# Kernel tuning notes

Measured on AMD Instinct MI355X. Metric: run time of the kernel, lower is better.

Reference implementation:

```python
import jax, jax.numpy as jnp
import numpy as np

DIM = 512
NUM_HEADS = 8
NUM_BLOCKS = 16
# NOTE: original code computes head_dim from FULL dim (before the reduce layer),
# so scale = (dim // num_heads) ** -0.5 = 64 ** -0.5, even though the actual
# per-head dim after reduce is 32. We preserve this quirk faithfully.
SCALE = (DIM // NUM_HEADS) ** -0.5


def setup_inputs() -> dict:
    key = jax.random.key(0)
    ks = jax.random.split(key, 5)
    B, N = 4, 4096
    C = DIM // 2
    x = jax.random.normal(ks[0], (B, N, DIM), dtype=jnp.float32)
    reduce_w = jax.random.normal(ks[1], (DIM, C), dtype=jnp.float32) * (DIM ** -0.5)
    qkv_w = jax.random.normal(ks[2], (C, 3 * C), dtype=jnp.float32) * (C ** -0.5)
    proj_w = jax.random.normal(ks[3], (C, DIM), dtype=jnp.float32) * (C ** -0.5)
    proj_b = jnp.zeros((DIM,), dtype=jnp.float32)
    return {"x": x, "reduce_w": reduce_w, "qkv_w": qkv_w,
            "proj_w": proj_w, "proj_b": proj_b}


def reference(x, reduce_w, qkv_w, proj_w, proj_b):
    B, N, _ = x.shape
    xr = x @ reduce_w                      # [B, N, C]  (C = dim/2)
    C = xr.shape[-1]
    H = NUM_HEADS
    d = C // H
    qkv = (xr @ qkv_w).reshape(B, N, 3, H, d).transpose(2, 0, 3, 1, 4)  # [3,B,H,N,d]
    q, k, v = qkv[0], qkv[1], qkv[2]
    bs = N // NUM_BLOCKS                   # block (chunk) size
    # block-diagonal local attention: reshape seq into independent blocks
    qb = q.reshape(B, H, NUM_BLOCKS, bs, d)
    kb = k.reshape(B, H, NUM_BLOCKS, bs, d)
    vb = v.reshape(B, H, NUM_BLOCKS, bs, d)
    attn = jnp.einsum('bhnqd,bhnkd->bhnqk', qb, kb) * SCALE
    attn = jax.nn.softmax(attn, axis=-1)
    ob = jnp.einsum('bhnqk,bhnkd->bhnqd', attn, vb)   # [B,H,Nb,bs,d]
    # torch: per-block transpose(1,2) then cat on dim=1 -> [B, N, H, d]
    o = ob.transpose(0, 2, 3, 1, 4).reshape(B, N, C)
    return o @ proj_w + proj_b
```

## Files before the change

kernel.cpp:

```cpp
#include <hip/hip_runtime.h>
#include <hip/hip_fp16.h>

typedef _Float16 half_t;
typedef _Float16 f16x8 __attribute__((ext_vector_type(8)));
typedef __fp16 fp16x2 __attribute__((ext_vector_type(2)));
typedef float f32x4 __attribute__((ext_vector_type(4)));

#define MFMA_F16(a, b, c) __builtin_amdgcn_mfma_f32_16x16x32_f16((a), (b), (c), 0, 0, 0)

static __device__ inline unsigned pkrtz(float a, float b) {
    union { fp16x2 h; unsigned u; } c;
    c.h = __builtin_amdgcn_cvt_pkrtz(a, b);
    return c.u;
}

__device__ __forceinline__ void gload16(const half_t* g, half_t* l) {
    __builtin_amdgcn_global_load_lds(
        (const __attribute__((address_space(1))) void*)g,
        (__attribute__((address_space(3))) void*)l, 16, 0, 0);
}

__global__ __launch_bounds__(256) void prep(
    const float* __restrict__ x, const float* __restrict__ qw,
    const float* __restrict__ rw, const float* __restrict__ pw,
    half_t* __restrict__ x_h, half_t* __restrict__ pw_t, half_t* __restrict__ Wt) {
    __shared__ __align__(16) char smem[24576];
    const int bid = blockIdx.x, tid = threadIdx.x;

    if (bid < 48) {
        char* As = smem;
        char* Bs = smem + 8192;
        const int M0 = (bid % 12) * 64, N0 = (bid / 12) * 128;
        const int lane = tid & 63, w = tid >> 6;
        const int l15 = lane & 15, l4 = lane >> 4;
        const int wrow = (w >> 1) * 32, wcol = (w & 1) * 64;
        const int pa = (l15 & 7) << 4;

        f32x4 acc[2][4];
#pragma unroll
        for (int i = 0; i < 2; ++i)
#pragma unroll
            for (int j = 0; j < 4; ++j) acc[i][j] = (f32x4){0.f, 0.f, 0.f, 0.f};

        for (int kc = 0; kc < 4; ++kc) {
            int c0 = kc * 64;
            __syncthreads();
#pragma unroll
            for (int i = 0; i < 2; ++i) {
                int j = tid + i * 256;
                int row = j >> 3, e8 = (j & 7) * 8;
                float s = (M0 + row) < 256 ? 0.125f : 1.f;
                f16x8 v;
#pragma unroll
                for (int e = 0; e < 8; ++e)
                    v[e] = (half_t)(qw[(size_t)(c0 + e8 + e) * 768 + M0 + row] * s);
                *(f16x8*)(As + row * 128 + ((e8 * 2) ^ ((row & 7) << 4))) = v;
            }
#pragma unroll
            for (int i = 0; i < 4; ++i) {
                int j = tid + i * 256;
                int row = j >> 3, e8 = (j & 7) * 8;
                const float* p = rw + (size_t)(N0 + row) * 256 + c0 + e8;
                float4 u0 = *(const float4*)p;
                float4 u1 = *(const float4*)(p + 4);
                f16x8 v;
                v[0] = (half_t)u0.x; v[1] = (half_t)u0.y;
                v[2] = (half_t)u0.z; v[3] = (half_t)u0.w;
                v[4] = (half_t)u1.x; v[5] = (half_t)u1.y;
                v[6] = (half_t)u1.z; v[7] = (half_t)u1.w;
                *(f16x8*)(Bs + row * 128 + ((e8 * 2) ^ ((row & 7) << 4))) = v;
            }
            __syncthreads();
#pragma unroll
            for (int ki = 0; ki < 2; ++ki) {
                f16x8 af[2], bf[4];
#pragma unroll
                for (int mi = 0; mi < 2; ++mi) {
                    int row = wrow + mi * 16 + l15;
                    af[mi] = *(const f16x8*)(As + row * 128 + (((ki * 4 + l4) << 4) ^ pa));
                }
#pragma unroll
                for (int nj = 0; nj < 4; ++nj) {
                    int row = wcol + nj * 16 + l15;
                    bf[nj] = *(const f16x8*)(Bs + row * 128 + (((ki * 4 + l4) << 4) ^ pa));
                }
#pragma unroll
                for (int mi = 0; mi < 2; ++mi)
#pragma unroll
                    for (int nj = 0; nj < 4; ++nj)
                        acc[mi][nj] = MFMA_F16(af[mi], bf[nj], acc[mi][nj]);
            }
        }
#pragma unroll
        for (int mi = 0; mi < 2; ++mi)
#pragma unroll
            for (int nj = 0; nj < 4; ++nj)
#pragma unroll
                for (int reg = 0; reg < 4; ++reg) {
                    int grow = M0 + wrow + mi * 16 + l4 * 4 + reg;
                    int gcol = N0 + wcol + nj * 16 + l15;
                    Wt[(size_t)grow * 512 + gcol] = (half_t)acc[mi][nj][reg];
                }
        return;
    }

    if (bid < 80) {
        half_t* tile = (half_t*)smem;
        int t = bid - 48;
        int R0 = (t >> 3) * 64, C0 = (t & 7) * 64;
#pragma unroll
        for (int e = 0; e < 16; ++e) {
            int idx = tid + e * 256;
            int r = idx >> 6, c = idx & 63;
            tile[r * 72 + c] = (half_t)pw[(size_t)(R0 + r) * 512 + C0 + c];
        }
        __syncthreads();
#pragma unroll
        for (int e = 0; e < 16; ++e) {
            int idx = tid + e * 256;
            int c = idx >> 6, r = idx & 63;
            pw_t[(size_t)(C0 + c) * 256 + R0 + r] = tile[r * 72 + c];
        }
        return;
    }

    int i8 = ((bid - 80) * 256 + tid) * 8;
    float4 a = *(const float4*)(x + i8);
    float4 b = *(const float4*)(x + i8 + 4);
    f16x8 v;
    v[0] = (half_t)a.x; v[1] = (half_t)a.y; v[2] = (half_t)a.z; v[3] = (half_t)a.w;
    v[4] = (half_t)b.x; v[5] = (half_t)b.y; v[6] = (half_t)b.z; v[7] = (half_t)b.w;
    *(f16x8*)(x_h + i8) = v;
}

template <int EPI, int K, int NB>
__global__ __launch_bounds__(256) void gemm_f16(
    const half_t* __restrict__ A, const half_t* __restrict__ Bt,
    void* __restrict__ Dst, const float* __restrict__ bias) {
    constexpr int nkt = K >> 6;
    constexpr int NLB = NB / 32;
    constexpr int NJ = NB / 32;
    constexpr int BUFSZ = 16384 + NB * 128;
    __shared__ __align__(16) char smem[2 * BUFSZ];

    const int tid = threadIdx.x;
    const int lane = tid & 63, w = tid >> 6;
    const int l15 = lane & 15, l4 = lane >> 4;
    const int wrow = (w >> 1) * 64, wcol = (w & 1) * (NB / 2);
    const int bm0 = blockIdx.x * 128;
    const int bn0 = blockIdx.y * NB;

    const half_t* srcA[4];
#pragma unroll
    for (int i = 0; i < 4; ++i) {
        int J = w * 256 + i * 64 + lane;
        int row = J >> 3, c = (J & 7) ^ (row & 7);
        srcA[i] = A + (size_t)(bm0 + row) * K + c * 8;
    }
    const half_t* srcB[NLB];
#pragma unroll
    for (int i = 0; i < NLB; ++i) {
        int J = w * (64 * NLB) + i * 64 + lane;
        int row = J >> 3, c = (J & 7) ^ (row & 7);
        srcB[i] = Bt + (size_t)(bn0 + row) * K + c * 8;
    }

    auto STAGE = [&](int kt) {
        char* As = smem + (kt & 1) * BUFSZ;
        char* Bs = As + 16384;
#pragma unroll
        for (int i = 0; i < 4; ++i)
            gload16(srcA[i] + kt * 64, (half_t*)(As + (w * 4 + i) * 1024));
#pragma unroll
        for (int i = 0; i < NLB; ++i)
            gload16(srcB[i] + kt * 64, (half_t*)(Bs + (w * NLB + i) * 1024));
    };

    f32x4 acc[4][NJ];
#pragma unroll
    for (int i = 0; i < 4; ++i)
#pragma unroll
        for (int j = 0; j < NJ; ++j) acc[i][j] = (f32x4){0.f, 0.f, 0.f, 0.f};

    const int pa = (l15 & 7) << 4;

    STAGE(0);
#pragma unroll
    for (int kt = 0; kt < nkt; ++kt) {
        if (kt + 1 < nkt) {
            STAGE(kt + 1);
            asm volatile("s_waitcnt vmcnt(%0)" ::"i"(4 + NLB) : "memory");
        } else {
            asm volatile("s_waitcnt vmcnt(0)" ::: "memory");
        }
        __builtin_amdgcn_s_barrier();
        __builtin_amdgcn_sched_barrier(0);

        const char* As = smem + (kt & 1) * BUFSZ;
        const char* Bs = As + 16384;
#pragma unroll
        for (int ki = 0; ki < 2; ++ki) {
            f16x8 af[4], bf[NJ];
#pragma unroll
            for (int mi = 0; mi < 4; ++mi) {
                int row = wrow + mi * 16 + l15;
                af[mi] = *(const f16x8*)(As + row * 128 + (((ki * 4 + l4) << 4) ^ pa));
            }
#pragma unroll
            for (int nj = 0; nj < NJ; ++nj) {
                int row = wcol + nj * 16 + l15;
                bf[nj] = *(const f16x8*)(Bs + row * 128 + (((ki * 4 + l4) << 4) ^ pa));
            }
#pragma unroll
            for (int mi = 0; mi < 4; ++mi)
#pragma unroll
                for (int nj = 0; nj < NJ; ++nj)
                    acc[mi][nj] = MFMA_F16(af[mi], bf[nj], acc[mi][nj]);
        }
        __builtin_amdgcn_sched_barrier(0);
        __builtin_amdgcn_s_barrier();
    }

#pragma unroll
    for (int mi = 0; mi < 4; ++mi) {
#pragma unroll
        for (int nj = 0; nj < NJ; ++nj) {
#pragma unroll
            for (int reg = 0; reg < 4; ++reg) {
                int grow = bm0 + wrow + mi * 16 + l4 * 4 + reg;
                int gcol = bn0 + wcol + nj * 16 + l15;
                float val = acc[mi][nj][reg];
                if (EPI == 1) {
                    int t = gcol >> 8, h = (gcol >> 5) & 7, dd = gcol & 31;
                    int b = grow >> 12, n = grow & 4095;
                    int blk = n >> 8, r = n & 255;
                    size_t base = (size_t)t * 4194304 +
                                  (size_t)((((b << 3) + h) << 4) + blk) * 8192;
                    size_t idx = (t == 2) ? base + (size_t)dd * 256 + r
                                          : base + (size_t)r * 32 + dd;
                    ((half_t*)Dst)[idx] = (half_t)val;
                } else {
                    ((float*)Dst)[(size_t)grow * 512 + gcol] = val + bias[gcol];
                }
            }
        }
    }
}

__global__ __launch_bounds__(512, 4) void attn_f16(const half_t* __restrict__ qkv_ws,
                                                   half_t* __restrict__ o_ws) {
    const int blkid = blockIdx.x;
    const int b = blkid >> 7, h = (blkid >> 4) & 7, blk = blkid & 15;
    const half_t* Q  = qkv_ws + (size_t)blkid * 8192;
    const half_t* Kp = qkv_ws + 4194304 + (size_t)blkid * 8192;
    const half_t* VT = qkv_ws + 8388608 + (size_t)blkid * 8192;

    const int tid = threadIdx.x, lane = tid & 63, w = tid >> 6;
    const int l15 = lane & 15, l4 = lane >> 4;
    const int qb = w * 32;

    f16x8 aq[2];
    aq[0] = *(const f16x8*)(Q + (qb + l15) * 32 + l4 * 8);
    aq[1] = *(const f16x8*)(Q + (qb + 16 + l15) * 32 + l4 * 8);

    float s_run[2] = {0.f, 0.f};
    f32x4 acc_o[2][2];
#pragma unroll
    for (int qg = 0; qg < 2; ++qg)
#pragma unroll
        for (int fo = 0; fo < 2; ++fo) acc_o[qg][fo] = (f32x4){0.f, 0.f, 0.f, 0.f};
    const f32x4 zero4 = (f32x4){0.f, 0.f, 0.f, 0.f};

    for (int kt = 0; kt < 4; ++kt) {
        f16x8 ka[4];
#pragma unroll
        for (int t = 0; t < 4; ++t)
            ka[t] = *(const f16x8*)(Kp + (kt * 64 + t * 16 + l15) * 32 + l4 * 8);
        f16x8 bv[2][2];
#pragma unroll
        for (int c = 0; c < 2; ++c)
#pragma unroll
            for (int fo = 0; fo < 2; ++fo)
                bv[c][fo] = *(const f16x8*)(VT + (fo * 16 + l15) * 256 + kt * 64 + c * 32 + l4 * 8);

        f32x4 st[2][4];
        __builtin_amdgcn_s_setprio(1);
#pragma unroll
        for (int qg = 0; qg < 2; ++qg)
#pragma unroll
            for (int t = 0; t < 4; ++t) st[qg][t] = MFMA_F16(ka[t], aq[qg], zero4);
        __builtin_amdgcn_s_setprio(0);

#pragma unroll
        for (int qg = 0; qg < 2; ++qg) {
            float p[4][4];
            float ps = 0.f;
#pragma unroll
            for (int t = 0; t < 4; ++t)
#pragma unroll
                for (int r = 0; r < 4; ++r) {
                    float e = __expf(st[qg][t][r]);
                    p[t][r] = e;
                    ps += e;
                }
            ps += __shfl_xor(ps, 16);
            ps += __shfl_xor(ps, 32);
            s_run[qg] += ps;

#pragma unroll
            for (int c = 0; c < 2; ++c) {
                unsigned pk0[2], pk1[2];
#pragma unroll
                for (int rp = 0; rp < 2; ++rp) {
                    pk0[rp] = pkrtz(p[2 * c][2 * rp], p[2 * c][2 * rp + 1]);
                    pk1[rp] = pkrtz(p[2 * c + 1][2 * rp], p[2 * c + 1][2 * rp + 1]);
                }
                union { unsigned u[4]; f16x8 v; } au;
#pragma unroll
                for (int j = 0; j < 4; ++j) {
                    int src = l15 + ((((l4 & 1) << 1) + (j >> 1)) << 4);
                    unsigned g0 = (unsigned)__shfl((int)pk0[j & 1], src);
                    unsigned g1 = (unsigned)__shfl((int)pk1[j & 1], src);
                    au.u[j] = (l4 < 2) ? g0 : g1;
                }
                __builtin_amdgcn_s_setprio(1);
#pragma unroll
                for (int fo = 0; fo < 2; ++fo)
                    acc_o[qg][fo] = MFMA_F16(au.v, bv[c][fo], acc_o[qg][fo]);
                __builtin_amdgcn_s_setprio(0);
            }
        }
    }

#pragma unroll
    for (int qg = 0; qg < 2; ++qg) {
        float inv = 1.f / s_run[qg];
        float sinv[4];
#pragma unroll
        for (int r = 0; r < 4; ++r) sinv[r] = __shfl(inv, (l4 << 2) | r);
#pragma unroll
        for (int fo = 0; fo < 2; ++fo)
#pragma unroll
            for (int r = 0; r < 4; ++r) {
                int grow = b * 4096 + blk * 256 + qb + qg * 16 + l4 * 4 + r;
                o_ws[(size_t)grow * 256 + h * 32 + fo * 16 + l15] =
                    (half_t)(acc_o[qg][fo][r] * sinv[r]);
            }
    }
}

extern "C" void kernel_launch(void* const* d_in, const int* in_sizes, int n_in,
                              void* d_out, int out_size, void* d_ws, size_t ws_size,
                              hipStream_t stream) {
    const float* x        = (const float*)d_in[0];
    const float* reduce_w = (const float*)d_in[1];
    const float* qkv_w    = (const float*)d_in[2];
    const float* proj_w   = (const float*)d_in[3];
    const float* proj_b   = (const float*)d_in[4];
    char* ws = (char*)d_ws;

    half_t* qkv_ws = (half_t*)ws;
    half_t* o_buf  = (half_t*)(ws + 25165824);
    half_t* pw_t   = (half_t*)(ws + 33554432);
    half_t* Wt     = (half_t*)(ws + 33816576);
    half_t* x_h    = (half_t*)(ws + 34603008);

    prep<<<4176, 256, 0, stream>>>(x, qkv_w, reduce_w, proj_w, x_h, pw_t, Wt);
    gemm_f16<1, 512, 192><<<dim3(128, 4), 256, 0, stream>>>(x_h, Wt, qkv_ws, nullptr);
    attn_f16<<<512, 512, 0, stream>>>(qkv_ws, o_buf);
    gemm_f16<2, 256, 128><<<dim3(128, 4), 256, 0, stream>>>(o_buf, pw_t, d_out, proj_b);
}
```

Before: 70.73 us.

## Retile GEMMs to 8 waves, transpose V in attention LDS, use exp2 softmax

The two GEMMs move from 4 to 8 waves per block, so each wave computes a narrower column slice. The hand-written vmcnt waits and split barriers are replaced by a single __syncthreads per k-step, and the MFMA section is wrapped in setprio. The QKV epilogue now writes V row-major like Q and K, and the attention kernel transposes V through padded shared memory instead of relying on a strided global store. The log2(e) factor is folded into the Q-weight scale so the softmax can use exp2f. The simpler synchronisation relies on the compiler waiting correctly for the global-to-LDS loads, which is a correctness risk, and it removes some of the explicit load/compute overlap.

```diff
diff --git a/kernel.cpp b/kernel.cpp
--- a/kernel.cpp
+++ b/kernel.cpp
@@ -14,7 +14,7 @@
     return c.u;
 }
 
-__device__ __forceinline__ void gload16(const half_t* g, half_t* l) {
+__device__ __forceinline__ void gload16(const half_t* g, char* l) {
     __builtin_amdgcn_global_load_lds(
         (const __attribute__((address_space(1))) void*)g,
         (__attribute__((address_space(3))) void*)l, 16, 0, 0);
@@ -23,7 +23,8 @@
 __global__ __launch_bounds__(256) void prep(
     const float* __restrict__ x, const float* __restrict__ qw,
     const float* __restrict__ rw, const float* __restrict__ pw,
-    half_t* __restrict__ x_h, half_t* __restrict__ pw_t, half_t* __restrict__ Wt) {
+    half_t* __restrict__ x_h, half_t* __restrict__ pw_t,
+    half_t* __restrict__ Wt) {
     __shared__ __align__(16) char smem[24576];
     const int bid = blockIdx.x, tid = threadIdx.x;
 
@@ -49,7 +50,7 @@
             for (int i = 0; i < 2; ++i) {
                 int j = tid + i * 256;
                 int row = j >> 3, e8 = (j & 7) * 8;
-                float s = (M0 + row) < 256 ? 0.125f : 1.f;
+                float s = (M0 + row) < 256 ? 0.18033688f : 1.f;
                 f16x8 v;
 #pragma unroll
                 for (int e = 0; e < 8; ++e)
@@ -133,34 +134,37 @@
     *(f16x8*)(x_h + i8) = v;
 }
 
-template <int EPI, int K, int NB>
-__global__ __launch_bounds__(256) void gemm_f16(
+template <int EPI, int NB, int K>
+__global__ __launch_bounds__(512) void gemm_f16(
     const half_t* __restrict__ A, const half_t* __restrict__ Bt,
     void* __restrict__ Dst, const float* __restrict__ bias) {
     constexpr int nkt = K >> 6;
-    constexpr int NLB = NB / 32;
-    constexpr int NJ = NB / 32;
+    constexpr int NAC = 2;
+    constexpr int NBC = NB / 64;
+    constexpr int NJ = NB / 64;
     constexpr int BUFSZ = 16384 + NB * 128;
     __shared__ __align__(16) char smem[2 * BUFSZ];
 
     const int tid = threadIdx.x;
     const int lane = tid & 63, w = tid >> 6;
     const int l15 = lane & 15, l4 = lane >> 4;
-    const int wrow = (w >> 1) * 64, wcol = (w & 1) * (NB / 2);
+    const int wrow = (w >> 2) * 64;
+    const int wcol = (w & 3) * (NB / 4);
     const int bm0 = blockIdx.x * 128;
     const int bn0 = blockIdx.y * NB;
-
-    const half_t* srcA[4];
-#pragma unroll
-    for (int i = 0; i < 4; ++i) {
-        int J = w * 256 + i * 64 + lane;
+    const int pa = (l15 & 7) << 4;
+
+    const half_t* srcA[NAC];
+#pragma unroll
+    for (int i = 0; i < NAC; ++i) {
+        int J = tid + i * 512;
         int row = J >> 3, c = (J & 7) ^ (row & 7);
         srcA[i] = A + (size_t)(bm0 + row) * K + c * 8;
     }
-    const half_t* srcB[NLB];
-#pragma unroll
-    for (int i = 0; i < NLB; ++i) {
-        int J = w * (64 * NLB) + i * 64 + lane;
+    const half_t* srcB[NBC];
+#pragma unroll
+    for (int i = 0; i < NBC; ++i) {
+        int J = tid + i * 512;
         int row = J >> 3, c = (J & 7) ^ (row & 7);
         srcB[i] = Bt + (size_t)(bn0 + row) * K + c * 8;
     }
@@ -169,11 +173,11 @@
         char* As = smem + (kt & 1) * BUFSZ;
         char* Bs = As + 16384;
 #pragma unroll
-        for (int i = 0; i < 4; ++i)
-            gload16(srcA[i] + kt * 64, (half_t*)(As + (w * 4 + i) * 1024));
-#pragma unroll
-        for (int i = 0; i < NLB; ++i)
-            gload16(srcB[i] + kt * 64, (half_t*)(Bs + (w * NLB + i) * 1024));
+        for (int i = 0; i < NAC; ++i)
+            gload16(srcA[i] + kt * 64, As + i * 8192 + w * 1024);
+#pragma unroll
+        for (int i = 0; i < NBC; ++i)
+            gload16(srcB[i] + kt * 64, Bs + i * 8192 + w * 1024);
     };
 
     f32x4 acc[4][NJ];
@@ -182,19 +186,10 @@
 #pragma unroll
         for (int j = 0; j < NJ; ++j) acc[i][j] = (f32x4){0.f, 0.f, 0.f, 0.f};
 
-    const int pa = (l15 & 7) << 4;
-
     STAGE(0);
-#pragma unroll
     for (int kt = 0; kt < nkt; ++kt) {
-        if (kt + 1 < nkt) {
-            STAGE(kt + 1);
-            asm volatile("s_waitcnt vmcnt(%0)" ::"i"(4 + NLB) : "memory");
-        } else {
-            asm volatile("s_waitcnt vmcnt(0)" ::: "memory");
-        }
-        __builtin_amdgcn_s_barrier();
-        __builtin_amdgcn_sched_barrier(0);
+        __syncthreads();
+        if (kt + 1 < nkt) STAGE(kt + 1);
 
         const char* As = smem + (kt & 1) * BUFSZ;
         const char* Bs = As + 16384;
@@ -211,14 +206,14 @@
                 int row = wcol + nj * 16 + l15;
                 bf[nj] = *(const f16x8*)(Bs + row * 128 + (((ki * 4 + l4) << 4) ^ pa));
             }
+            __builtin_amdgcn_s_setprio(1);
 #pragma unroll
             for (int mi = 0; mi < 4; ++mi)
 #pragma unroll
                 for (int nj = 0; nj < NJ; ++nj)
                     acc[mi][nj] = MFMA_F16(af[mi], bf[nj], acc[mi][nj]);
-        }
-        __builtin_amdgcn_sched_barrier(0);
-        __builtin_amdgcn_s_barrier();
+            __builtin_amdgcn_s_setprio(0);
+        }
     }
 
 #pragma unroll
@@ -234,10 +229,9 @@
                     int t = gcol >> 8, h = (gcol >> 5) & 7, dd = gcol & 31;
                     int b = grow >> 12, n = grow & 4095;
                     int blk = n >> 8, r = n & 255;
-                    size_t base = (size_t)t * 4194304 +
-                                  (size_t)((((b << 3) + h) << 4) + blk) * 8192;
-                    size_t idx = (t == 2) ? base + (size_t)dd * 256 + r
-                                          : base + (size_t)r * 32 + dd;
+                    size_t idx = (size_t)t * 4194304 +
+                                 (size_t)((((b << 3) + h) << 4) + blk) * 8192 +
+                                 (size_t)r * 32 + dd;
                     ((half_t*)Dst)[idx] = (half_t)val;
                 } else {
                     ((float*)Dst)[(size_t)grow * 512 + gcol] = val + bias[gcol];
@@ -249,20 +243,33 @@
 
 __global__ __launch_bounds__(512, 4) void attn_f16(const half_t* __restrict__ qkv_ws,
                                                    half_t* __restrict__ o_ws) {
+    __shared__ __align__(16) half_t VT[32 * 264];
+
     const int blkid = blockIdx.x;
     const int b = blkid >> 7, h = (blkid >> 4) & 7, blk = blkid & 15;
     const half_t* Q  = qkv_ws + (size_t)blkid * 8192;
     const half_t* Kp = qkv_ws + 4194304 + (size_t)blkid * 8192;
-    const half_t* VT = qkv_ws + 8388608 + (size_t)blkid * 8192;
+    const half_t* V  = qkv_ws + 8388608 + (size_t)blkid * 8192;
 
     const int tid = threadIdx.x, lane = tid & 63, w = tid >> 6;
     const int l15 = lane & 15, l4 = lane >> 4;
     const int qb = w * 32;
 
+#pragma unroll
+    for (int i = 0; i < 2; ++i) {
+        int c = tid + i * 512;
+        int key = c >> 2, k8 = (c & 3) * 8;
+        f16x8 v = *(const f16x8*)(V + key * 32 + k8);
+#pragma unroll
+        for (int e = 0; e < 8; ++e) VT[(k8 + e) * 264 + key] = v[e];
+    }
+
     f16x8 aq[2];
     aq[0] = *(const f16x8*)(Q + (qb + l15) * 32 + l4 * 8);
     aq[1] = *(const f16x8*)(Q + (qb + 16 + l15) * 32 + l4 * 8);
 
+    __syncthreads();
+
     float s_run[2] = {0.f, 0.f};
     f32x4 acc_o[2][2];
 #pragma unroll
@@ -281,7 +288,7 @@
         for (int c = 0; c < 2; ++c)
 #pragma unroll
             for (int fo = 0; fo < 2; ++fo)
-                bv[c][fo] = *(const f16x8*)(VT + (fo * 16 + l15) * 256 + kt * 64 + c * 32 + l4 * 8);
+                bv[c][fo] = *(const f16x8*)&VT[(fo * 16 + l15) * 264 + kt * 64 + c * 32 + l4 * 8];
 
         f32x4 st[2][4];
         __builtin_amdgcn_s_setprio(1);
@@ -299,7 +306,7 @@
             for (int t = 0; t < 4; ++t)
 #pragma unroll
                 for (int r = 0; r < 4; ++r) {
-                    float e = __expf(st[qg][t][r]);
+                    float e = exp2f(st[qg][t][r]);
                     p[t][r] = e;
                     ps += e;
                 }
@@ -366,7 +373,7 @@
     half_t* x_h    = (half_t*)(ws + 34603008);
 
     prep<<<4176, 256, 0, stream>>>(x, qkv_w, reduce_w, proj_w, x_h, pw_t, Wt);
-    gemm_f16<1, 512, 192><<<dim3(128, 4), 256, 0, stream>>>(x_h, Wt, qkv_ws, nullptr);
+    gemm_f16<1, 192, 512><<<dim3(128, 4), 512, 0, stream>>>(x_h, Wt, qkv_ws, nullptr);
     attn_f16<<<512, 512, 0, stream>>>(qkv_ws, o_buf);
-    gemm_f16<2, 256, 128><<<dim3(128, 4), 256, 0, stream>>>(o_buf, pw_t, d_out, proj_b);
-}
+    gemm_f16<2, 128, 256><<<dim3(128, 4), 512, 0, stream>>>(o_buf, pw_t, d_out, proj_b);
+}
```

After: 64.37 us. -9.0%, faster.
